# Kernel optimization log

Measured on AMD Instinct MI355X. Metric: run time of the kernel, lower is better.

The kernel has to match this reference:

```python
import jax, jax.numpy as jnp
import numpy as np
from jax import lax

NH = 8  # heads


def _ln(x, g, b):
    m = x.mean(-1, keepdims=True)
    v = ((x - m) ** 2).mean(-1, keepdims=True)
    return (x - m) * lax.rsqrt(v + 1e-5) * g + b


def _pos_idx(n):
    # torch: linspace(n-1,0,n)[:,None] + linspace(0,n-1,n)[None,:], flattened long
    r = np.linspace(n - 1, 0, n).reshape(n, 1)
    c = np.linspace(0, n - 1, n).reshape(1, n)
    return jnp.asarray((r + c).reshape(-1).astype(np.int32))


def _mha(q_in, k_in, v_in, in_w, in_b, out_w, out_b, pos_enc=None, pos_idx=None, attn_mask=None):
    # MultiheadAttentionRelative: q/k/v proj + relative pos-encoding gather terms
    w, bsz, e = q_in.shape
    hd = e // NH
    scale = hd ** -0.5
    q = (q_in @ in_w[:e].T + in_b[:e]) * scale
    k = k_in @ in_w[e:2 * e].T + in_b[e:2 * e]
    v = v_in @ in_w[2 * e:].T + in_b[2 * e:]
    q = q.reshape(w, bsz, NH, hd)
    k = k.reshape(w, bsz, NH, hd)
    v = v.reshape(w, bsz, NH, hd)
    attn = jnp.einsum('wnec,vnec->newv', q, k)  # [N,E,W,W']
    if pos_enc is not None:
        pe = pos_enc[pos_idx].reshape(w, w, e)  # [2W-1,C] -> [W,W',C] gather
        q_r = ((pe @ in_w[:e].T + in_b[:e]) * scale).reshape(w, w, NH, hd)
        k_r = (pe @ in_w[e:2 * e].T + in_b[e:2 * e]).reshape(w, w, NH, hd)
        attn = attn + jnp.einsum('wnec,wvec->newv', q, k_r) + jnp.einsum('vnec,wvec->newv', k, q_r)
    if attn_mask is not None:
        attn = attn + attn_mask[None, None]
    raw = attn
    p = jax.nn.softmax(attn, axis=-1)
    v_o = jnp.einsum('newv,vnec->wnec', p, v).reshape(w, bsz, e)
    return v_o @ out_w.T + out_b, raw.sum(axis=1)


def _interp_lin(x, out_size):
    # torch F.interpolate(mode='linear', align_corners=False) along last axis
    L_in = x.shape[-1]
    if L_in == out_size:
        return x
    coords = jnp.clip((jnp.arange(out_size, dtype=jnp.float32) + 0.5) * (L_in / out_size) - 0.5, 0.0, L_in - 1.0)
    lo = jnp.floor(coords).astype(jnp.int32)
    hi = jnp.minimum(lo + 1, L_in - 1)
    frac = coords - lo.astype(jnp.float32)
    return x[..., lo] * (1.0 - frac) + x[..., hi] * frac


def _conv(x, w, b, pad):
    y = lax.conv_general_dilated(x, w, (1, 1), pad, dimension_numbers=('NCHW', 'OIHW', 'NCHW'))
    return y + b[None, :, None, None]


def _self_layer(feat, feat1, pos, pidx, pos1, pidx1, posy, pidxy, posy1, pidxy1, p):
    iw, ib, ow, ob, n1g, n1b, n2g, n2b = p
    f2 = _ln(feat, n1g, n1b)
    f4 = _ln(feat1, n2g, n2b)
    w_, h2, c = f2.shape
    w1_, h4, c1 = f4.shape
    # row<->col switch: [W,2HN,C] -> [HN,2W,C]
    f2y = jnp.transpose(f2.reshape(w_, 2, h2 // 2, c), (2, 1, 0, 3)).reshape(h2 // 2, 2 * w_, c)
    f4y = jnp.transpose(f4.reshape(w1_, 2, h4 // 2, c1), (2, 1, 0, 3)).reshape(h4 // 2, 2 * w1_, c1)
    f2y, _ = _mha(f2y, f2y, f2y, iw[1], ib[1], ow[1], ob[1], posy, pidxy)
    f2 = jnp.transpose(f2y.reshape(h2 // 2, 2, w_, c), (2, 1, 0, 3)).reshape(w_, h2, c)
    f4y, _ = _mha(f4y, f4y, f4y, iw[3], ib[3], ow[3], ob[3], posy1, pidxy1)
    f4 = jnp.transpose(f4y.reshape(h4 // 2, 2, w1_, c1), (2, 1, 0, 3)).reshape(w1_, h4, c1)
    f2, _ = _mha(f2, f2, f2, iw[0], ib[0], ow[0], ob[0], pos, pidx)
    f4, _ = _mha(f4, f4, f4, iw[2], ib[2], ow[2], ob[2], pos1, pidx1)
    return feat + f2, feat1 + f4


def _cross_layer(fl, fr, fl1, fr1, pos, pidx, pos1, pidx1, p, last):
    iw, ib, ow, ob, n1g, n1b, n2g, n2b, mw1, mb1, mw2, mb2 = p
    fl2 = _ln(fl, n1g, n1b)
    fr2 = _ln(fr, n1g, n1b)
    fl4 = _ln(fl1, n2g, n2b)
    fr4 = _ln(fr1, n2g, n2b)
    up_r, _ = _mha(fr2, fl2, fl2, iw[0], ib[0], ow[0], ob[0], jnp.flip(pos, 0), pidx)
    up_r1, _ = _mha(fr4, fl4, fl4, iw[1], ib[1], ow[1], ob[1], jnp.flip(pos1, 0), pidx1)
    fr = fr + up_r
    fr1n = fr1 + up_r1
    if last:
        w = fl2.shape[0]
        w1 = fl4.shape[0]
        m = jnp.where(jnp.triu(jnp.ones((w, w), jnp.float32), 1) == 1.0, -jnp.inf, 0.0)
        m1 = jnp.where(jnp.triu(jnp.ones((w1, w1), jnp.float32), 1) == 1.0, -jnp.inf, 0.0)
    else:
        m = None
        m1 = None
    fr2n = _ln(fr, n1g, n1b)
    up_l, raw = _mha(fl2, fr2n, fr2n, iw[0], ib[0], ow[0], ob[0], pos, pidx, m)
    fr4n = _ln(fr1n, n2g, n2b)
    up_l1, _ = _mha(fl4, fr4n, fr4n, iw[1], ib[1], ow[1], ob[1], pos1, pidx1, m1)
    fl = fl + up_l
    fl1n = fl1 + up_l1
    feat = jnp.concatenate([fl, fr], 1)        # [W,2HN,C]
    feat_n = jnp.concatenate([fl1n, fr1n], 1)  # [W1,2HN,C]
    x = jnp.transpose(feat_n, (2, 1, 0))       # [C,2HN,W1]
    x = _interp_lin(x, feat.shape[0])          # [C,2HN,W]
    feat_n = jnp.transpose(x, (2, 1, 0))
    feat_n = jnp.concatenate([feat_n, feat], 2)  # [W,2HN,2C]
    x = jnp.transpose(feat_n, (2, 1, 0))[None]   # [1,2C,2HN,W]
    x = _conv(x, mw1, mb1, 'VALID')
    x = _conv(x, mw2, mb2, ((1, 1), (1, 1)))
    out = jnp.transpose(x[0], (2, 1, 0))         # [W,2HN,C]
    return out, raw


def reference(feat_left, feat_right, feat_left1, feat_right1, pos_enc, pos_enc1, pos_enc_y, pos_enc_y1,
              sa_in_w, sa_in_b, sa_out_w, sa_out_b, sa_n1_g, sa_n1_b, sa_n2_g, sa_n2_b,
              ca_in_w, ca_in_b, ca_out_w, ca_out_b, ca_n1_g, ca_n1_b, ca_n2_g, ca_n2_b,
              merge_w1, merge_b1, merge_w2, merge_b2):
    bs, c, h, w = feat_left.shape
    w1 = feat_left1.shape[3]
    hn = h * bs

    def flat(x):
        return jnp.transpose(x, (3, 2, 0, 1)).reshape(x.shape[3], -1, c)  # [W,HN,C]

    fl, fr = flat(feat_left), flat(feat_right)
    fl1, fr1 = flat(feat_left1), flat(feat_right1)
    pidx = _pos_idx(w)
    pidx1 = _pos_idx(w1)
    pidxy = _pos_idx(hn)
    pidxy1 = _pos_idx(hn)
    feat = jnp.concatenate([fl, fr], 1)    # [W,2HN,C]
    feat1 = jnp.concatenate([fl1, fr1], 1)  # [W1,2HN,C]
    L = sa_in_w.shape[0]
    raw = None
    for i in range(L):
        sp = (sa_in_w[i], sa_in_b[i], sa_out_w[i], sa_out_b[i], sa_n1_g[i], sa_n1_b[i], sa_n2_g[i], sa_n2_b[i])
        feat, feat1 = _self_layer(feat, feat1, pos_enc, pidx, pos_enc1, pidx1, pos_enc_y, pidxy, pos_enc_y1, pidxy1, sp)
        cp = (ca_in_w[i], ca_in_b[i], ca_out_w[i], ca_out_b[i], ca_n1_g[i], ca_n1_b[i], ca_n2_g[i], ca_n2_b[i],
              merge_w1[i], merge_b1[i], merge_w2[i], merge_b2[i])
        feat, raw = _cross_layer(feat[:, :hn], feat[:, hn:], feat1[:, :hn], feat1[:, hn:],
                                 pos_enc, pidx, pos_enc1, pidx1, cp, i == L - 1)
    attn_weight = jnp.transpose(raw.reshape(h, bs, w, w), (1, 0, 2, 3))  # [N,H,W,W]
    return attn_weight


def setup_inputs() -> dict:
    key = jax.random.key(0)
    ks = iter(jax.random.split(key, 40))
    N, C, H, W, W1, Lyr = 1, 128, 64, 128, 64, 6
    s = 0.05
    d = {}
    d['feat_left'] = jax.random.normal(next(ks), (N, C, H, W), jnp.float32)
    d['feat_right'] = jax.random.normal(next(ks), (N, C, H, W), jnp.float32)
    d['feat_left1'] = jax.random.normal(next(ks), (N, C, H, W1), jnp.float32)
    d['feat_right1'] = jax.random.normal(next(ks), (N, C, H, W1), jnp.float32)
    d['pos_enc'] = jax.random.normal(next(ks), (2 * W - 1, C), jnp.float32) * 0.1
    d['pos_enc1'] = jax.random.normal(next(ks), (2 * W1 - 1, C), jnp.float32) * 0.1
    d['pos_enc_y'] = jax.random.normal(next(ks), (2 * H - 1, C), jnp.float32) * 0.1
    d['pos_enc_y1'] = jax.random.normal(next(ks), (2 * H - 1, C), jnp.float32) * 0.1
    d['sa_in_w'] = jax.random.normal(next(ks), (Lyr, 4, 3 * C, C), jnp.float32) * s
    d['sa_in_b'] = jnp.zeros((Lyr, 4, 3 * C), jnp.float32)
    d['sa_out_w'] = jax.random.normal(next(ks), (Lyr, 4, C, C), jnp.float32) * s
    d['sa_out_b'] = jnp.zeros((Lyr, 4, C), jnp.float32)
    d['sa_n1_g'] = jnp.ones((Lyr, C), jnp.float32)
    d['sa_n1_b'] = jnp.zeros((Lyr, C), jnp.float32)
    d['sa_n2_g'] = jnp.ones((Lyr, C), jnp.float32)
    d['sa_n2_b'] = jnp.zeros((Lyr, C), jnp.float32)
    d['ca_in_w'] = jax.random.normal(next(ks), (Lyr, 2, 3 * C, C), jnp.float32) * s
    d['ca_in_b'] = jnp.zeros((Lyr, 2, 3 * C), jnp.float32)
    d['ca_out_w'] = jax.random.normal(next(ks), (Lyr, 2, C, C), jnp.float32) * s
    d['ca_out_b'] = jnp.zeros((Lyr, 2, C), jnp.float32)
    d['ca_n1_g'] = jnp.ones((Lyr, C), jnp.float32)
    d['ca_n1_b'] = jnp.zeros((Lyr, C), jnp.float32)
    d['ca_n2_g'] = jnp.ones((Lyr, C), jnp.float32)
    d['ca_n2_b'] = jnp.zeros((Lyr, C), jnp.float32)
    d['merge_w1'] = jax.random.normal(next(ks), (Lyr, 128, 256, 1, 1), jnp.float32) * s
    d['merge_b1'] = jnp.zeros((Lyr, 128), jnp.float32)
    d['merge_w2'] = jax.random.normal(next(ks), (Lyr, 128, 128, 3, 3), jnp.float32) * s
    d['merge_b2'] = jnp.zeros((Lyr, 128), jnp.float32)
    return d
```

## Files before the change

kernel.cpp:

```cpp
#include <hip/hip_runtime.h>
#include <hip/hip_bf16.h>
#include <math.h>


typedef __attribute__((ext_vector_type(8))) short bf16x8;
typedef __attribute__((ext_vector_type(4))) float f32x4;
typedef __hip_bfloat16 bf16;

__device__ __forceinline__ float b2f(unsigned short u) {
  return __uint_as_float((unsigned)u << 16);
}
__device__ __forceinline__ short f2bs(float x) {
  bf16 h = __float2bfloat16(x);
  short s;
  __builtin_memcpy(&s, &h, 2);
  return s;
}
__device__ __forceinline__ int ymap(int t, int D0, int D1) {
  return (t % D0) * (2 * D1) + ((t / D0) & 1) * D1 + t / (2 * D0);
}


__global__ void k_build_feat(const float* __restrict__ L, const float* __restrict__ R,
                             float* __restrict__ feat, int W) {
  int t = blockIdx.x;
  int c = threadIdx.x;
  int b = t & 127;
  int w = t >> 7;
  const float* src = (b < 64) ? L : R;
  int h = b & 63;
  feat[(size_t)t * 128 + c] = src[((size_t)c * 64 + h) * W + w];
}

struct FDesc { const float* s; bf16* d; int n; };
struct FArgs { FDesc d[9]; int cum[10]; int nprob; };
__global__ void k_f2b_multi(FArgs fa) {
  int bid = blockIdx.x;
  int p = 0;
  while (p + 1 < fa.nprob && bid >= fa.cum[p + 1]) ++p;
  const FDesc d = fa.d[p];
  int i = (bid - fa.cum[p]) * 1024 + threadIdx.x * 4;
  if (i + 3 < d.n) {
    float4 x = *(const float4*)(d.s + i);
    d.d[i + 0] = __float2bfloat16(x.x);
    d.d[i + 1] = __float2bfloat16(x.y);
    d.d[i + 2] = __float2bfloat16(x.z);
    d.d[i + 3] = __float2bfloat16(x.w);
  } else {
    for (int z = 0; z < 4 && i + z < d.n; ++z) d.d[i + z] = __float2bfloat16(d.s[i + z]);
  }
}

__global__ void k_wfullb(const float* __restrict__ w2, bf16* __restrict__ wf) {
  int bid = blockIdx.x;
  int l = bid >> 7, co = bid & 127;
  int ci = threadIdx.x;
  const float* src = w2 + (size_t)l * 128 * 128 * 9;
  bf16* dst = wf + (size_t)l * 128 * 1152;
#pragma unroll
  for (int ky = 0; ky < 3; ky++)
#pragma unroll
    for (int kx = 0; kx < 3; kx++)
      dst[(size_t)co * 1152 + (kx * 3 + ky) * 128 + ci] =
          __float2bfloat16(src[((size_t)(co * 128 + ci) * 3 + ky) * 3 + kx]);
}

__global__ void k_zero_guard(bf16* p0, bf16* p1) {
  int t = threadIdx.x;
  p0[255 * 256 + t] = __float2bfloat16(0.0f);
  p1[127 * 256 + t] = __float2bfloat16(0.0f);
}

struct WCArgs { const bf16* iw[12]; const bf16* ow[12]; bf16* out[12]; };
__global__ __launch_bounds__(256) void k_wcomb(WCArgs a) {
  __shared__ bf16 sOw[128 * 128];
  int p = blockIdx.x / 6, rc = blockIdx.x % 6;
  const bf16* iw = a.iw[p];
  const bf16* ow = a.ow[p];
  for (int i = threadIdx.x; i < 128 * 16; i += 256)
    ((bf16x8*)sOw)[i] = ((const bf16x8*)ow)[i];
  __syncthreads();
  int row = rc * 64 + (threadIdx.x >> 2);
  int seg = (threadIdx.x & 3) * 32;
  float acc[32];
#pragma unroll
  for (int c = 0; c < 32; ++c) acc[c] = 0.f;
  for (int t = 0; t < 128; ++t) {
    float av = b2f((unsigned short)iw[row * 128 + t]);
#pragma unroll
    for (int c = 0; c < 32; ++c)
      acc[c] = fmaf(av, b2f((unsigned short)sOw[t * 128 + seg + c]), acc[c]);
  }
  bf16* o = a.out[p] + (size_t)row * 128 + seg;
  for (int c = 0; c < 32; ++c) o[c] = __float2bfloat16(acc[c]);
}

struct BCArgs { const float* iwf[12]; const float* obf[12]; const float* ibf[12]; float* out[12]; };
__global__ void k_bcomb(BCArgs a) {
  int p = blockIdx.x, j = threadIdx.x;
  const float* iw = a.iwf[p] + (size_t)j * 128;
  const float* ob = a.obf[p];
  float acc = a.ibf[p][j];
  for (int t = 0; t < 128; ++t) acc = fmaf(iw[t], ob[t], acc);
  a.out[p][j] = acc;
}


struct LDesc { const float* src; bf16* dst; const float* g; const float* be;
               int ntok, Bout, PBin, offIn; };
struct LArgs { LDesc d[4]; int cum[5]; int nprob; };

__global__ __launch_bounds__(256) void k_ln_multi(LArgs la) {
  int bid = blockIdx.x;
  int p = 0;
  while (p + 1 < la.nprob && bid >= la.cum[p + 1]) ++p;
  const LDesc d = la.d[p];
  int t = (bid - la.cum[p]) * 4 + (threadIdx.x >> 6);
  int lane = threadIdx.x & 63;
  if (t >= d.ntok) return;
  int w = t / d.Bout, b = t - w * d.Bout;
  const float* row = d.src + (size_t)(w * d.PBin + d.offIn + b) * 128;
  float x0 = row[lane], x1 = row[lane + 64];
  float s = x0 + x1;
#pragma unroll
  for (int o = 32; o; o >>= 1) s += __shfl_xor(s, o, 64);
  float m = s * (1.0f / 128.0f);
  float d0 = x0 - m, d1 = x1 - m;
  float v = d0 * d0 + d1 * d1;
#pragma unroll
  for (int o = 32; o; o >>= 1) v += __shfl_xor(v, o, 64);
  float r = 1.0f / sqrtf(v * (1.0f / 128.0f) + 1e-5f);
  bf16* orow = d.dst + (size_t)t * 128;
  orow[lane]      = __float2bfloat16(d0 * r * d.g[lane]      + d.be[lane]);
  orow[lane + 64] = __float2bfloat16(d1 * r * d.g[lane + 64] + d.be[lane + 64]);
}


struct GDesc {
  const bf16* A; const float* Af0; const float* Af1;
  const bf16* W; const float* bias;
  bf16* Cb; float* Cf; const float* resid;
  int M, N, K, lda, scaleN;
  int imode, iD0, iD1;
  int omode, oD0, oD1, ooff;
};
struct GArgs { GDesc d[6]; int cum[7]; int nprob; };

__global__ __launch_bounds__(256) void k_gemm_multi(GArgs ga) {
  __shared__ bf16x8 sA[64 * 4];
  __shared__ bf16x8 sB[64 * 4];
  int bid = blockIdx.x;
  int p = 0;
  while (p + 1 < ga.nprob && bid >= ga.cum[p + 1]) ++p;
  const GDesc d = ga.d[p];
  int local = bid - ga.cum[p];
  int tilesx = d.N >> 6;
  int ty = local / tilesx, tx = local - ty * tilesx;
  const int m0 = ty << 6, n0 = tx << 6;
  const int tid = threadIdx.x;
  const int lane = tid & 63;
  const int wave = tid >> 6;
  const int wm = wave >> 1, wn = wave & 1;
  const int fr = lane & 15;
  const int kc = lane >> 4;
  f32x4 acc[2][2];
#pragma unroll
  for (int f = 0; f < 2; f++)
#pragma unroll
    for (int g = 0; g < 2; g++) acc[f][g] = (f32x4){0.f, 0.f, 0.f, 0.f};

  for (int k0 = 0; k0 < d.K; k0 += 32) {
    {
      int row = tid >> 2, ch = tid & 3;
      int m = m0 + row;
      bf16x8 val = (bf16x8){0, 0, 0, 0, 0, 0, 0, 0};
      if (d.imode == 0) {
        if (m < d.M) val = *(const bf16x8*)(d.A + (size_t)m * d.lda + k0 + ch * 8);
      } else if (d.imode == 1) {
        if (m < d.M) {
          int ar = ymap(m, d.iD0, d.iD1);
          val = *(const bf16x8*)(d.A + (size_t)ar * d.lda + k0 + ch * 8);
        }
      } else if (d.imode == 2) {
        int kblk = k0 >> 7;
        int kx = kblk / 3, ky = kblk - kx * 3;
        int arow = m + (kx - 1) * 128;
        int y = (m & 127) + (ky - 1);
        if (arow >= 0 && arow < d.M && y >= 0 && y < 128)
          val = *(const bf16x8*)(d.A + (size_t)arow * d.lda + (k0 & 127) + ch * 8);
      } else {
        int kk = k0 + ch * 8;
        int w = m >> 7, y = m & 127;
        if (kk < 128) {
          float xo = fminf(fmaxf(w * 0.5f - 0.25f, 0.0f), 63.0f);
          int lo = (int)xo;
          int hi = (lo + 1 < 63) ? lo + 1 : 63;
          float f = xo - (float)lo;
          const float* a0 = d.Af0 + ((size_t)lo * 128 + y) * 128 + kk;
          const float* a1 = d.Af0 + ((size_t)hi * 128 + y) * 128 + kk;
#pragma unroll
          for (int z = 0; z < 8; ++z) val[z] = f2bs(a0[z] * (1.0f - f) + a1[z] * f);
        } else {
          const float* a0 = d.Af1 + (size_t)m * 128 + (kk - 128);
#pragma unroll
          for (int z = 0; z < 8; ++z) val[z] = f2bs(a0[z]);
        }
      }
      sA[row * 4 + (ch ^ ((row >> 2) & 3))] = val;
      bf16x8 bval = *(const bf16x8*)(d.W + (size_t)(n0 + row) * d.K + k0 + ch * 8);
      sB[row * 4 + (ch ^ ((row >> 2) & 3))] = bval;
    }
    __syncthreads();
    bf16x8 af[2], bg[2];
#pragma unroll
    for (int f = 0; f < 2; ++f) {
      int row = wm * 32 + f * 16 + fr;
      af[f] = sA[row * 4 + (kc ^ ((row >> 2) & 3))];
    }
#pragma unroll
    for (int g = 0; g < 2; ++g) {
      int row = wn * 32 + g * 16 + fr;
      bg[g] = sB[row * 4 + (kc ^ ((row >> 2) & 3))];
    }
#pragma unroll
    for (int f = 0; f < 2; ++f)
#pragma unroll
      for (int g = 0; g < 2; ++g)
        acc[f][g] = __builtin_amdgcn_mfma_f32_16x16x32_bf16(af[f], bg[g], acc[f][g], 0, 0, 0);
    __syncthreads();
  }
  const int r4 = (lane >> 4) << 2;
  const int ocol = lane & 15;
#pragma unroll
  for (int f = 0; f < 2; ++f) {
#pragma unroll
    for (int g = 0; g < 2; ++g) {
      int n = n0 + wn * 32 + g * 16 + ocol;
      float bv = d.bias ? d.bias[n] : 0.0f;
      bool sc = (n < d.scaleN);
#pragma unroll
      for (int i = 0; i < 4; ++i) {
        int m = m0 + wm * 32 + f * 16 + r4 + i;
        if (m < d.M) {
          int row;
          if (d.omode == 0) row = (m / d.oD0) * d.oD1 + d.ooff + (m % d.oD0);
          else row = ymap(m, d.oD0, d.oD1);
          size_t idx = (size_t)row * d.N + n;
          float val = acc[f][g][i] + bv;
          if (sc) val *= 0.25f;
          if (d.resid) val += d.resid[idx];
          if (d.Cb) d.Cb[idx] = __float2bfloat16(val);
          else d.Cf[idx] = val;
        }
      }
    }
  }
}


struct ADesc {
  const bf16* Q; const bf16* K; const bf16* V;
  const bf16* PPb; bf16* O;
  int ldQ, ldK, ldV, Wlen, B, sflip, useMask;
};
struct AArgs { ADesc d[2]; int cum[3]; int nprob; };

template<int WLEN, int SGN>
__device__ __forceinline__ void attn_core(const ADesc& d, int b, int st, int h,
                                          int tid, bf16* smem) {
  constexpr int NT = WLEN / 16;
  constexpr int R = WLEN - 1;
  constexpr int PST = WLEN + 8;
  const f32x4 z4 = (f32x4){0.f, 0.f, 0.f, 0.f};
  const bf16x8 zb = (bf16x8){0, 0, 0, 0, 0, 0, 0, 0};
  bf16* Vt  = smem;
  bf16* Pl  = smem + 64 * PST;
  bf16* T2l = smem + 128 * PST;
  bf16* Ost = T2l + 1280;

  {
    int q = tid & (WLEN / 2 - 1);
    int cc = tid >> ((WLEN == 128) ? 6 : 5);
    constexpr int CH = (WLEN == 128) ? 16 : 8;
    int cb = cc * CH;
    const bf16* v0p = d.V + ((size_t)(2 * q) * d.B + b) * d.ldV + h * 64 + cb;
    const bf16* v1p = d.V + ((size_t)(2 * q + 1) * d.B + b) * d.ldV + h * 64 + cb;
#pragma unroll
    for (int j = 0; j < CH; j += 8) {
      bf16x8 a = *(const bf16x8*)(v0p + j);
      bf16x8 bb = *(const bf16x8*)(v1p + j);
#pragma unroll
      for (int z = 0; z < 8; ++z) {
        unsigned pk = (unsigned)(unsigned short)a[z] |
                      ((unsigned)(unsigned short)bb[z] << 16);
        *(unsigned*)(Vt + (size_t)(cb + j + z) * PST + 2 * q) = pk;
      }
    }
  }
  __syncthreads();

  const int wave = tid >> 6, l = tid & 63;
  const int lm = l & 15, lg = l >> 4;
  const bool zlane = (lg >= 2);
  bf16* Pw  = Pl + wave * (16 * PST);
  bf16* T2w = T2l + wave * (16 * 20);
  int p0[4], src[4], hi[4], tsel[4];
  bool csel[4];
#pragma unroll
  for (int i = 0; i < 4; ++i) {
    p0[i] = SGN * (lm - 4 * lg - i) + 15;
    src[i] = (l & 48) | (p0[i] & 15);
    hi[i] = p0[i] & 16;
    if (SGN == 1) {
      int t0 = lm + 15 - 4 * lg - i;
      csel[i] = (t0 < 16);
      tsel[i] = csel[i] ? t0 : t0 - 16;
    } else {
      int t0 = lm - 15 + 4 * lg + i;
      csel[i] = (t0 >= 0);
      tsel[i] = csel[i] ? t0 : t0 + 16;
    }
  }

  const int w0 = st * 16;
  const int chb = h * 64 + wave * 16 + lg * 8;

  bf16x8 qf = zb;
  if (!zlane) qf = *(const bf16x8*)(d.Q + ((size_t)(w0 + lm) * d.B + b) * d.ldQ + chb);

  const int U0 = (SGN == 1) ? (R - w0 - 15) : (R + w0 - WLEN + 1);
  const int Ub0 = (SGN == 1) ? (R - w0 - 15) : (R - (WLEN - 16) + w0 - 15);
  const bf16* t1p = d.PPb + (size_t)(U0 + lm) * 256 + 128 + chb;
  const bf16* t2p = d.PPb + (size_t)(Ub0 + lm) * 256 + chb;
  const int v0i = ((SGN == 1) ? 0 : (WLEN - 16)) + lm;
  const bf16* kp = d.K + ((size_t)v0i * d.B + b) * d.ldK + chb;
  const ptrdiff_t kstep = (ptrdiff_t)SGN * 16 * d.B * d.ldK;

  f32x4 t1a;
  {
    bf16x8 z = zb;
    if (!zlane) z = *(const bf16x8*)t1p;
    t1p += 16 * 256;
    t1a = __builtin_amdgcn_mfma_f32_16x16x32_bf16(qf, z, z4, 0, 0, 0);
  }
  int v = v0i;
#pragma unroll
  for (int j = 0; j < NT; ++j) {
    f32x4 t1b;
    {
      bf16x8 z = zb;
      if (!zlane) z = *(const bf16x8*)t1p;
      t1p += 16 * 256;
      t1b = __builtin_amdgcn_mfma_f32_16x16x32_bf16(qf, z, z4, 0, 0, 0);
    }
    bf16x8 kf = zb;
    if (!zlane) kf = *(const bf16x8*)kp;
    kp += kstep;
    f32x4 s4 = __builtin_amdgcn_mfma_f32_16x16x32_bf16(qf, kf, z4, 0, 0, 0);
    bf16x8 zA = zb, zB = zb;
    if (!zlane) {
      zA = *(const bf16x8*)t2p;
      zB = *(const bf16x8*)(t2p + 16 * 256);
    }
    t2p += 16 * 256;
    f32x4 t2A = __builtin_amdgcn_mfma_f32_16x16x32_bf16(zA, kf, z4, 0, 0, 0);
    f32x4 t2B = __builtin_amdgcn_mfma_f32_16x16x32_bf16(zB, kf, z4, 0, 0, 0);
#pragma unroll
    for (int i = 0; i < 4; ++i)
      T2w[lm * 20 + tsel[i]] = f2bs(csel[i] ? t2A[i] : t2B[i]);
    ushort4 t2u = *(const ushort4*)(T2w + lm * 20 + 4 * lg);
    unsigned short t2a[4] = {t2u.x, t2u.y, t2u.z, t2u.w};
#pragma unroll
    for (int i = 0; i < 4; ++i) {
      float va = __shfl(t1a[i], src[i], 64);
      float vb = __shfl(t1b[i], src[i], 64);
      float s = s4[i] + (hi[i] ? vb : va) + b2f(t2a[i]);
      Pw[(4 * lg + i) * PST + v] = f2bs(__expf(s));
    }
    t1a = t1b;
    v += SGN * 16;
  }
  const bf16x8 ones = (bf16x8){0x3F80, 0x3F80, 0x3F80, 0x3F80,
                               0x3F80, 0x3F80, 0x3F80, 0x3F80};
  f32x4 oa = z4, rsm = z4;
#pragma unroll
  for (int vc = 0; vc < NT / 2; ++vc) {
    bf16x8 pf = *(const bf16x8*)(Pw + lm * PST + vc * 32 + lg * 8);
    bf16x8 vf = *(const bf16x8*)(Vt + (size_t)(wave * 16 + lm) * PST + vc * 32 + lg * 8);
    oa = __builtin_amdgcn_mfma_f32_16x16x32_bf16(pf, vf, oa, 0, 0, 0);
    rsm = __builtin_amdgcn_mfma_f32_16x16x32_bf16(pf, ones, rsm, 0, 0, 0);
  }
#pragma unroll
  for (int i = 0; i < 4; ++i)
    Ost[(4 * lg + i) * 80 + wave * 16 + lm] = f2bs(oa[i] / rsm[i]);
  __syncthreads();
  if (tid < 128) {
    int row = tid >> 3, ch8 = (tid & 7) * 8;
    bf16x8 vv = *(const bf16x8*)(Ost + row * 80 + ch8);
    *(bf16x8*)(d.O + ((size_t)(w0 + row) * d.B + b) * 128 + h * 64 + ch8) = vv;
  }
}

__global__ __launch_bounds__(256, 4) void k_attn_mfma(AArgs aa) {
  extern __shared__ bf16 smem[];
  int bid = blockIdx.x;
  int p = 0;
  while (p + 1 < aa.nprob && bid >= aa.cum[p + 1]) ++p;
  const ADesc d = aa.d[p];
  int local = bid - aa.cum[p];
  int b = local % d.B;
  int rest = local / d.B;
  int ns = d.Wlen >> 4;
  int st = rest % ns, h = rest / ns;
  int tid = threadIdx.x;
  if (d.Wlen == 128) {
    if (d.sflip == 1) attn_core<128, 1>(d, b, st, h, tid, smem);
    else attn_core<128, -1>(d, b, st, h, tid, smem);
  } else {
    if (d.sflip == 1) attn_core<64, 1>(d, b, st, h, tid, smem);
    else attn_core<64, -1>(d, b, st, h, tid, smem);
  }
}

__global__ __launch_bounds__(256, 2) void k_attn_raw(ADesc d) {
  __shared__ bf16 T2l[4 * 16 * 20];
  __shared__ float Rl[4][16][128];
  constexpr int NT = 8;
  constexpr int R = 127;
  const f32x4 z4 = (f32x4){0.f, 0.f, 0.f, 0.f};
  const bf16x8 zb = (bf16x8){0, 0, 0, 0, 0, 0, 0, 0};
  int bid = blockIdx.x;
  int b = bid % d.B, st = bid / d.B;
  int tid = threadIdx.x;
  const int wave = tid >> 6, l = tid & 63;
  const int lm = l & 15, lg = l >> 4;
  const bool zlane = (lg >= 2);
  bf16* T2w = T2l + wave * (16 * 20);
  int p0[4];
#pragma unroll
  for (int i = 0; i < 4; ++i) p0[i] = (lm - 4 * lg - i) + 15;
  const int w0 = st * 16;
  f32x4 raw[NT];
#pragma unroll
  for (int vt = 0; vt < NT; ++vt) raw[vt] = z4;

  for (int hh = 0; hh < 2; ++hh) {
    const int e = wave * 2 + hh;
    const int chb = e * 16 + lg * 8;
    bf16x8 qf = zb;
    if (!zlane) qf = *(const bf16x8*)(d.Q + ((size_t)(w0 + lm) * d.B + b) * d.ldQ + chb);
    const int U0 = R - w0 - 15;
    f32x4 t1a;
    {
      int u = min(max(U0 + lm, 0), 2 * R);
      bf16x8 z = zb;
      if (!zlane) z = *(const bf16x8*)(d.PPb + (size_t)u * 256 + 128 + chb);
      t1a = __builtin_amdgcn_mfma_f32_16x16x32_bf16(qf, z, z4, 0, 0, 0);
    }
#pragma unroll
    for (int j = 0; j < NT; ++j) {
      const int vt = j;
      const int v = vt * 16 + lm;
      f32x4 t1b;
      {
        int u = min(max(U0 + (j + 1) * 16 + lm, 0), 2 * R);
        bf16x8 z = zb;
        if (!zlane) z = *(const bf16x8*)(d.PPb + (size_t)u * 256 + 128 + chb);
        t1b = __builtin_amdgcn_mfma_f32_16x16x32_bf16(qf, z, z4, 0, 0, 0);
      }
      bf16x8 kf = zb;
      if (!zlane) kf = *(const bf16x8*)(d.K + ((size_t)v * d.B + b) * d.ldK + chb);
      f32x4 s4 = __builtin_amdgcn_mfma_f32_16x16x32_bf16(qf, kf, z4, 0, 0, 0);
      const int Ub = R + vt * 16 - w0 - 15;
#pragma unroll
      for (int u2 = 0; u2 < 2; ++u2) {
        int ua = min(max(Ub + u2 * 16 + lm, 0), 2 * R);
        bf16x8 z = zb;
        if (!zlane) z = *(const bf16x8*)(d.PPb + (size_t)ua * 256 + chb);
        f32x4 t2 = __builtin_amdgcn_mfma_f32_16x16x32_bf16(z, kf, z4, 0, 0, 0);
#pragma unroll
        for (int i = 0; i < 4; ++i) {
          int u = Ub + u2 * 16 + 4 * lg + i;
          int t = R + v - u - w0;
          if (t >= 0 && t < 16) T2w[lm * 20 + t] = f2bs(t2[i]);
        }
      }
      ushort4 t2u = *(const ushort4*)(T2w + lm * 20 + 4 * lg);
      unsigned short t2a[4] = {t2u.x, t2u.y, t2u.z, t2u.w};
#pragma unroll
      for (int i = 0; i < 4; ++i) {
        int src = (l & 48) | (p0[i] & 15);
        float va = __shfl(t1a[i], src, 64);
        float vb = __shfl(t1b[i], src, 64);
        float s = s4[i] + ((p0[i] & 16) ? vb : va) + b2f(t2a[i]);
        if (v > (w0 + 4 * lg + i)) s = -INFINITY;
        raw[vt][i] += s;
      }
      t1a = t1b;
    }
  }
#pragma unroll
  for (int vt = 0; vt < NT; ++vt)
#pragma unroll
    for (int i = 0; i < 4; ++i)
      Rl[wave][4 * lg + i][vt * 16 + lm] = raw[vt][i];
  __syncthreads();
  {
    int r = tid >> 4, v8 = (tid & 15) * 8;
    int w = w0 + r;
    bf16* out = d.O + ((size_t)b * 128 + w) * 128;
#pragma unroll
    for (int z = 0; z < 8; ++z) {
      int vv = v8 + z;
      float sum = Rl[0][r][vv] + Rl[1][r][vv] + Rl[2][r][vv] + Rl[3][r][vv];
      out[vv] = __float2bfloat16((vv > w) ? 0.0f : sum);
    }
  }
}


extern "C" void kernel_launch(void* const* d_in, const int* in_sizes, int n_in,
                              void* d_out, int out_size, void* d_ws, size_t ws_size,
                              hipStream_t stream) {
  (void)in_sizes; (void)n_in; (void)out_size; (void)ws_size;
  const float* FLt  = (const float*)d_in[0];
  const float* FRt  = (const float*)d_in[1];
  const float* FL1t = (const float*)d_in[2];
  const float* FR1t = (const float*)d_in[3];
  const float* PE   = (const float*)d_in[4];
  const float* PE1  = (const float*)d_in[5];
  const float* PEY  = (const float*)d_in[6];
  const float* PEY1 = (const float*)d_in[7];
  const float* SA_IW = (const float*)d_in[8];
  const float* SA_IB = (const float*)d_in[9];
  const float* SA_OW = (const float*)d_in[10];
  const float* SA_OB = (const float*)d_in[11];
  const float* SA_N1G = (const float*)d_in[12];
  const float* SA_N1B = (const float*)d_in[13];
  const float* SA_N2G = (const float*)d_in[14];
  const float* SA_N2B = (const float*)d_in[15];
  const float* CA_IW = (const float*)d_in[16];
  const float* CA_IB = (const float*)d_in[17];
  const float* CA_OW = (const float*)d_in[18];
  const float* CA_OB = (const float*)d_in[19];
  const float* CA_N1G = (const float*)d_in[20];
  const float* CA_N1B = (const float*)d_in[21];
  const float* CA_N2G = (const float*)d_in[22];
  const float* CA_N2B = (const float*)d_in[23];
  const float* MW1 = (const float*)d_in[24];
  const float* MB1 = (const float*)d_in[25];
  const float* MW2 = (const float*)d_in[26];
  const float* MB2 = (const float*)d_in[27];

  float* ws = (float*)d_ws;
  float* FEAT  = ws;
  float* FEAT1 = ws + 2097152;
  float* FN2   = ws + 3145728;
  bf16* PP0b   = (bf16*)(ws + 4194304);
  bf16* PP1b   = (bf16*)(ws + 4259840);
  float* B2f   = ws + 4276224;
  bf16* hb = (bf16*)(ws + 4292608);
  bf16* QKV   = hb;
  bf16* QKV1  = hb + 6291456;
  bf16* Xb    = hb + 9437184;
  bf16* XBb   = hb + 11534336;
  bf16* Ob    = hb + 12582912;
  bf16* Ob1   = hb + 14680064;
  bf16* PEb   = hb + 15728640;
  bf16* PE1b  = hb + 15761408;
  bf16* PEYb  = hb + 15777792;
  bf16* PEY1b = hb + 15794176;
  bf16* SAIWb = hb + 15810560;
  bf16* SAOWb = hb + 18169856;
  bf16* CAIWb = hb + 18563072;
  bf16* CAOWb = hb + 19742720;
  bf16* MW1b  = hb + 19939328;
  bf16* WFb   = hb + 20135936;
  bf16* W2b   = hb + 21020672;

  bf16* QR   = QKV + 3145728;
  bf16* FL4F = QKV + 4194304;
  bf16* QR1  = QKV + 5767168;
  bf16* KVq  = QKV1;
  bf16* KVq1 = QKV1 + 2097152;
  bf16* XR2  = Xb;
  bf16* XR21 = Xb + 1048576;

  GArgs ga; int ng = 0; int gb = 0;
  auto gadd = [&](GDesc gd) { ga.cum[ng] = gb; ga.d[ng] = gd;
                              gb += ((gd.M + 63) >> 6) * (gd.N >> 6); ++ng; };
  auto gflush = [&]() { ga.nprob = ng;
                        k_gemm_multi<<<gb, 256, 0, stream>>>(ga); ng = 0; gb = 0; };
  LArgs la; int nl = 0; int lb = 0;
  auto lnadd = [&](LDesc ld) { la.cum[nl] = lb; la.d[nl] = ld;
                               lb += (ld.ntok + 3) / 4; ++nl; };
  auto lnflush = [&]() { la.nprob = nl;
                         k_ln_multi<<<lb, 256, 0, stream>>>(la); nl = 0; lb = 0; };
  AArgs aa; int na = 0; int ab = 0; int maxw = 0;
  auto aadd = [&](ADesc ad) { aa.cum[na] = ab; aa.d[na] = ad;
                              ab += ad.B * (ad.Wlen >> 4) * 2;
                              if (ad.Wlen > maxw) maxw = ad.Wlen; ++na; };
  auto aflush = [&]() { aa.nprob = na;
                        size_t sh = (size_t)(128 * (maxw + 8) + 2560) * 2;
                        k_attn_mfma<<<ab, 256, sh, stream>>>(aa);
                        na = 0; ab = 0; maxw = 0; };

  auto G = [&](const bf16* A, const bf16* W, const float* bias,
               bf16* Cb, float* Cf, const float* resid,
               int M, int N, int K, int lda, int scaleN,
               int imode, int iD0, int iD1,
               int omode, int oD0, int oD1, int ooff,
               const float* Af0 = nullptr, const float* Af1 = nullptr) {
    GDesc gd; gd.A = A; gd.Af0 = Af0; gd.Af1 = Af1; gd.W = W; gd.bias = bias;
    gd.Cb = Cb; gd.Cf = Cf; gd.resid = resid;
    gd.M = M; gd.N = N; gd.K = K; gd.lda = lda; gd.scaleN = scaleN;
    gd.imode = imode; gd.iD0 = iD0; gd.iD1 = iD1;
    gd.omode = omode; gd.oD0 = oD0; gd.oD1 = oD1; gd.ooff = ooff;
    gadd(gd);
  };
  auto AT = [&](const bf16* Q, int ldQ, const bf16* K, int ldK, const bf16* V, int ldV,
                const bf16* PPb, int Wlen, int B, int sflip, bf16* O) {
    ADesc ad; ad.Q = Q; ad.K = K; ad.V = V; ad.PPb = PPb; ad.O = O;
    ad.ldQ = ldQ; ad.ldK = ldK; ad.ldV = ldV; ad.Wlen = Wlen; ad.B = B;
    ad.sflip = sflip; ad.useMask = 0;
    aadd(ad);
  };

  {
    FArgs fa; int nf = 0; int fb = 0;
    auto fadd = [&](const float* s, bf16* dd, int n) {
      fa.cum[nf] = fb; fa.d[nf] = FDesc{s, dd, n}; fb += (n + 1023) / 1024; ++nf; };
    fadd(SA_IW, SAIWb, 6 * 4 * 384 * 128);
    fadd(SA_OW, SAOWb, 6 * 4 * 128 * 128);
    fadd(CA_IW, CAIWb, 6 * 2 * 384 * 128);
    fadd(CA_OW, CAOWb, 6 * 2 * 128 * 128);
    fadd(MW1,   MW1b,  6 * 128 * 256);
    fadd(PE,    PEb,   255 * 128);
    fadd(PE1,   PE1b,  127 * 128);
    fadd(PEY,   PEYb,  127 * 128);
    fadd(PEY1,  PEY1b, 127 * 128);
    fa.nprob = nf;
    k_f2b_multi<<<fb, 256, 0, stream>>>(fa);
  }
  k_wfullb<<<768, 128, 0, stream>>>(MW2, WFb);
  k_zero_guard<<<1, 256, 0, stream>>>(PP0b, PP1b);
  {
    WCArgs wc; BCArgs bc;
    for (int l = 0; l < 6; ++l) {
      for (int s = 0; s < 2; ++s) {
        int p = l * 2 + s;
        int iwi = (s == 0) ? 0 : 2;
        int owi = (s == 0) ? 1 : 3;
        wc.iw[p]  = SAIWb + (size_t)l * 4 * 384 * 128 + (size_t)iwi * 384 * 128;
        wc.ow[p]  = SAOWb + (size_t)l * 4 * 128 * 128 + (size_t)owi * 128 * 128;
        wc.out[p] = W2b + (size_t)p * 384 * 128;
        bc.iwf[p] = SA_IW + (size_t)l * 4 * 384 * 128 + (size_t)iwi * 384 * 128;
        bc.obf[p] = SA_OB + (size_t)l * 4 * 128 + (size_t)owi * 128;
        bc.ibf[p] = SA_IB + (size_t)l * 4 * 384 + (size_t)iwi * 384;
        bc.out[p] = B2f + (size_t)p * 384;
      }
    }
    k_wcomb<<<72, 256, 0, stream>>>(wc);
    k_bcomb<<<12, 384, 0, stream>>>(bc);
  }
  k_build_feat<<<16384, 128, 0, stream>>>(FLt, FRt, FEAT, 128);
  k_build_feat<<<8192, 128, 0, stream>>>(FL1t, FR1t, FEAT1, 64);

  for (int l = 0; l < 6; ++l) {
    bool last = (l == 5);
    const bf16* iw  = SAIWb + (size_t)l * 4 * 384 * 128;
    const float* ib = SA_IB + (size_t)l * 4 * 384;
    const bf16* ow  = SAOWb + (size_t)l * 4 * 128 * 128;
    const float* ob = SA_OB + (size_t)l * 4 * 128;
    const bf16* ciw  = CAIWb + (size_t)l * 2 * 384 * 128;
    const float* cib = CA_IB + (size_t)l * 2 * 384;
    const bf16* cow  = CAOWb + (size_t)l * 2 * 128 * 128;
    const float* cob = CA_OB + (size_t)l * 2 * 128;
    const bf16* ciw1 = ciw + 384 * 128;
    const float* cib1 = cib + 384;
    const bf16* cow1 = cow + 128 * 128;
    const float* cob1 = cob + 128;
    const int IW = 384 * 128, OW = 128 * 128;

    lnadd(LDesc{FEAT, Xb, SA_N1G + l * 128, SA_N1B + l * 128, 16384, 128, 128, 0});
    if (!last) lnadd(LDesc{FEAT1, XBb, SA_N2G + l * 128, SA_N2B + l * 128, 8192, 128, 128, 0});
    lnflush();
    G(Xb, iw + IW, ib + 384, QKV, nullptr, nullptr, 16384, 384, 128, 128, 128, 1, 128, 64, 0, 1, 1, 0);
    if (!last) G(XBb, iw + 3 * IW, ib + 3 * 384, QKV1, nullptr, nullptr, 8192, 384, 128, 128, 128, 1, 64, 64, 0, 1, 1, 0);
    G(PEYb, iw + IW, ib + 384, PP0b, nullptr, nullptr, 127, 256, 128, 128, 128, 0, 0, 0, 0, 1, 1, 0);
    if (!last) G(PEY1b, iw + 3 * IW, ib + 3 * 384, PP1b, nullptr, nullptr, 127, 256, 128, 128, 128, 0, 0, 0, 0, 1, 1, 0);
    gflush();
    AT(QKV, 384, QKV + 128, 384, QKV + 256, 384, PP0b, 64, 256, 1, Ob);
    if (!last) AT(QKV1, 384, QKV1 + 128, 384, QKV1 + 256, 384, PP1b, 64, 128, 1, Ob1);
    aflush();
    G(Ob, W2b + (size_t)(l * 2) * 49152, B2f + (l * 2) * 384, QKV, nullptr, nullptr,
      16384, 384, 128, 128, 128, 1, 64, 128, 0, 1, 1, 0);
    if (!last) G(Ob1, W2b + (size_t)(l * 2 + 1) * 49152, B2f + (l * 2 + 1) * 384, QKV1,
                 nullptr, nullptr, 8192, 384, 128, 128, 128, 1, 64, 64, 0, 1, 1, 0);
    G(PEb, iw, ib, PP0b, nullptr, nullptr, 255, 256, 128, 128, 128, 0, 0, 0, 0, 1, 1, 0);
    if (!last) G(PE1b, iw + 2 * IW, ib + 2 * 384, PP1b, nullptr, nullptr, 127, 256, 128, 128, 128, 0, 0, 0, 0, 1, 1, 0);
    gflush();
    AT(QKV, 384, QKV + 128, 384, QKV + 256, 384, PP0b, 128, 128, 1, Ob);
    if (!last) AT(QKV1, 384, QKV1 + 128, 384, QKV1 + 256, 384, PP1b, 64, 128, 1, Ob1);
    aflush();
    G(Ob, ow, ob, nullptr, FEAT, FEAT, 16384, 128, 128, 128, 0, 0, 0, 0, 0, 1, 1, 0);
    if (!last) G(Ob1, ow + 2 * OW, ob + 2 * 128, nullptr, FEAT1, FEAT1, 8192, 128, 128, 128, 0, 0, 0, 0, 0, 1, 1, 0);
    gflush();

    lnadd(LDesc{FEAT, Xb, CA_N1G + l * 128, CA_N1B + l * 128, 8192, 64, 128, 0});
    lnadd(LDesc{FEAT, Xb + 1048576, CA_N1G + l * 128, CA_N1B + l * 128, 8192, 64, 128, 64});
    if (!last) {
      lnadd(LDesc{FEAT1, XBb, CA_N2G + l * 128, CA_N2B + l * 128, 4096, 64, 128, 0});
      lnadd(LDesc{FEAT1, XBb + 524288, CA_N2G + l * 128, CA_N2B + l * 128, 4096, 64, 128, 64});
    }
    lnflush();
    G(Xb, ciw, cib, QKV, nullptr, nullptr, 8192, 384, 128, 128, 128, 0, 0, 0, 0, 1, 1, 0);
    G(Xb + 1048576, ciw, cib, QR, nullptr, nullptr, 8192, 128, 128, 128, 128, 0, 0, 0, 0, 1, 1, 0);
    if (!last) {
      G(XBb, ciw1, cib1, FL4F, nullptr, nullptr, 4096, 384, 128, 128, 128, 0, 0, 0, 0, 1, 1, 0);
      G(XBb + 524288, ciw1, cib1, QR1, nullptr, nullptr, 4096, 128, 128, 128, 128, 0, 0, 0, 0, 1, 1, 0);
    }
    G(PEb, ciw, cib, PP0b, nullptr, nullptr, 255, 256, 128, 128, 128, 0, 0, 0, 0, 1, 1, 0);
    if (!last) G(PE1b, ciw1, cib1, PP1b, nullptr, nullptr, 127, 256, 128, 128, 128, 0, 0, 0, 0, 1, 1, 0);
    gflush();
    AT(QR, 128, QKV + 128, 384, QKV + 256, 384, PP0b, 128, 64, -1, Ob);
    if (!last) AT(QR1, 128, FL4F + 128, 384, FL4F + 256, 384, PP1b, 64, 64, -1, Ob1);
    aflush();
    G(Ob, cow, cob, nullptr, FEAT, FEAT, 8192, 128, 128, 128, 0, 0, 0, 0, 0, 64, 128, 64);
    if (!last) G(Ob1, cow1, cob1, nullptr, FN2, FEAT1, 4096, 128, 128, 128, 0, 0, 0, 0, 0, 64, 128, 64);
    gflush();
    lnadd(LDesc{FEAT, XR2, CA_N1G + l * 128, CA_N1B + l * 128, 8192, 64, 128, 64});
    if (!last) lnadd(LDesc{FN2, XR21, CA_N2G + l * 128, CA_N2B + l * 128, 4096, 64, 128, 64});
    lnflush();
    G(XR2, ciw + 128 * 128, cib + 128, KVq, nullptr, nullptr, 8192, 256, 128, 128, 0, 0, 0, 0, 0, 1, 1, 0);
    if (!last) G(XR21, ciw1 + 128 * 128, cib1 + 128, KVq1, nullptr, nullptr, 4096, 256, 128, 128, 0, 0, 0, 0, 0, 1, 1, 0);
    gflush();
    if (last) {
      ADesc ad; ad.Q = QKV; ad.K = KVq; ad.V = KVq + 128; ad.PPb = PP0b;
      ad.O = (bf16*)d_out;
      ad.ldQ = 384; ad.ldK = 256; ad.ldV = 256;
      ad.Wlen = 128; ad.B = 64; ad.sflip = 1; ad.useMask = 1;
      k_attn_raw<<<64 * 8, 256, 0, stream>>>(ad);
      break;
    }
    AT(QKV, 384, KVq, 256, KVq + 128, 256, PP0b, 128, 64, 1, Ob);
    AT(FL4F, 384, KVq1, 256, KVq1 + 128, 256, PP1b, 64, 64, 1, Ob1);
    aflush();
    G(Ob, cow, cob, nullptr, FEAT, FEAT, 8192, 128, 128, 128, 0, 0, 0, 0, 0, 64, 128, 0);
    G(Ob1, cow1, cob1, nullptr, FN2, FEAT1, 4096, 128, 128, 128, 0, 0, 0, 0, 0, 64, 128, 0);
    gflush();
    G(nullptr, MW1b + (size_t)l * 128 * 256, MB1 + l * 128, Ob, nullptr, nullptr,
      16384, 128, 256, 256, 0, 3, 0, 0, 0, 1, 1, 0, FN2, FEAT);
    gflush();
    G(Ob, WFb + (size_t)l * 128 * 1152, MB2 + l * 128, nullptr, FEAT, nullptr,
      16384, 128, 1152, 128, 0, 2, 0, 0, 0, 1, 1, 0);
    gflush();
  }
}
```

Measured before the change: 1.593 ms.

## Fuse LayerNorm into GEMM A-operand loading and drop separate LN kernel

Removes the standalone multi-problem LayerNorm kernel and its bf16 intermediate buffers. The GEMM gains a new input mode that computes per-row mean and rstd in shared memory from the fp32 source, then normalizes and converts to bf16 while loading A tiles. This saves kernel launches and a write/read round trip of the normalized activations. In exchange, every N-tile block recomputes the row statistics and rereads the fp32 source, and it uses a one-pass variance formula.

```diff
diff --git a/kernel.cpp b/kernel.cpp
--- a/kernel.cpp
+++ b/kernel.cpp
@@ -106,42 +106,13 @@
 }
 
 
-struct LDesc { const float* src; bf16* dst; const float* g; const float* be;
-               int ntok, Bout, PBin, offIn; };
-struct LArgs { LDesc d[4]; int cum[5]; int nprob; };
-
-__global__ __launch_bounds__(256) void k_ln_multi(LArgs la) {
-  int bid = blockIdx.x;
-  int p = 0;
-  while (p + 1 < la.nprob && bid >= la.cum[p + 1]) ++p;
-  const LDesc d = la.d[p];
-  int t = (bid - la.cum[p]) * 4 + (threadIdx.x >> 6);
-  int lane = threadIdx.x & 63;
-  if (t >= d.ntok) return;
-  int w = t / d.Bout, b = t - w * d.Bout;
-  const float* row = d.src + (size_t)(w * d.PBin + d.offIn + b) * 128;
-  float x0 = row[lane], x1 = row[lane + 64];
-  float s = x0 + x1;
-#pragma unroll
-  for (int o = 32; o; o >>= 1) s += __shfl_xor(s, o, 64);
-  float m = s * (1.0f / 128.0f);
-  float d0 = x0 - m, d1 = x1 - m;
-  float v = d0 * d0 + d1 * d1;
-#pragma unroll
-  for (int o = 32; o; o >>= 1) v += __shfl_xor(v, o, 64);
-  float r = 1.0f / sqrtf(v * (1.0f / 128.0f) + 1e-5f);
-  bf16* orow = d.dst + (size_t)t * 128;
-  orow[lane]      = __float2bfloat16(d0 * r * d.g[lane]      + d.be[lane]);
-  orow[lane + 64] = __float2bfloat16(d1 * r * d.g[lane + 64] + d.be[lane + 64]);
-}
-
-
 struct GDesc {
   const bf16* A; const float* Af0; const float* Af1;
   const bf16* W; const float* bias;
   bf16* Cb; float* Cf; const float* resid;
+  const float* lnsrc; const float* lng; const float* lnbe;
   int M, N, K, lda, scaleN;
-  int imode, iD0, iD1;
+  int imode, iD0, iD1, lnOff, lnYmap;
   int omode, oD0, oD1, ooff;
 };
 struct GArgs { GDesc d[6]; int cum[7]; int nprob; };
@@ -149,6 +120,8 @@
 __global__ __launch_bounds__(256) void k_gemm_multi(GArgs ga) {
   __shared__ bf16x8 sA[64 * 4];
   __shared__ bf16x8 sB[64 * 4];
+  __shared__ float sMean[64];
+  __shared__ float sRstd[64];
   int bid = blockIdx.x;
   int p = 0;
   while (p + 1 < ga.nprob && bid >= ga.cum[p + 1]) ++p;
@@ -163,6 +136,31 @@
   const int wm = wave >> 1, wn = wave & 1;
   const int fr = lane & 15;
   const int kc = lane >> 4;
+
+  if (d.imode == 5) {
+    int row = tid >> 2, q = tid & 3;
+    int m = m0 + row;
+    int r = d.lnYmap ? ymap(m, d.iD0, d.iD1)
+                     : (m / d.iD0) * d.iD1 + d.lnOff + (m % d.iD0);
+    const float* src = d.lnsrc + (size_t)r * 128 + q * 32;
+    float s = 0.f, ss = 0.f;
+#pragma unroll
+    for (int j = 0; j < 32; j += 4) {
+      float4 x = *(const float4*)(src + j);
+      s += x.x + x.y + x.z + x.w;
+      ss += x.x * x.x + x.y * x.y + x.z * x.z + x.w * x.w;
+    }
+    s += __shfl_xor(s, 1, 64); s += __shfl_xor(s, 2, 64);
+    ss += __shfl_xor(ss, 1, 64); ss += __shfl_xor(ss, 2, 64);
+    if (q == 0) {
+      float mean = s * (1.0f / 128.0f);
+      float var = fmaxf(ss * (1.0f / 128.0f) - mean * mean, 0.0f);
+      sMean[row] = mean;
+      sRstd[row] = 1.0f / sqrtf(var + 1e-5f);
+    }
+    __syncthreads();
+  }
+
   f32x4 acc[2][2];
 #pragma unroll
   for (int f = 0; f < 2; f++)
@@ -188,6 +186,16 @@
         int y = (m & 127) + (ky - 1);
         if (arow >= 0 && arow < d.M && y >= 0 && y < 128)
           val = *(const bf16x8*)(d.A + (size_t)arow * d.lda + (k0 & 127) + ch * 8);
+      } else if (d.imode == 5) {
+        int r = d.lnYmap ? ymap(m, d.iD0, d.iD1)
+                         : (m / d.iD0) * d.iD1 + d.lnOff + (m % d.iD0);
+        const float* a0 = d.lnsrc + (size_t)r * 128 + k0 + ch * 8;
+        const float* gg = d.lng + k0 + ch * 8;
+        const float* bb = d.lnbe + k0 + ch * 8;
+        float mean = sMean[row], rstd = sRstd[row];
+#pragma unroll
+        for (int z = 0; z < 8; ++z)
+          val[z] = f2bs((a0[z] - mean) * rstd * gg[z] + bb[z]);
       } else {
         int kk = k0 + ch * 8;
         int w = m >> 7, y = m & 127;
@@ -562,8 +570,6 @@
   bf16* hb = (bf16*)(ws + 4292608);
   bf16* QKV   = hb;
   bf16* QKV1  = hb + 6291456;
-  bf16* Xb    = hb + 9437184;
-  bf16* XBb   = hb + 11534336;
   bf16* Ob    = hb + 12582912;
   bf16* Ob1   = hb + 14680064;
   bf16* PEb   = hb + 15728640;
@@ -583,19 +589,12 @@
   bf16* QR1  = QKV + 5767168;
   bf16* KVq  = QKV1;
   bf16* KVq1 = QKV1 + 2097152;
-  bf16* XR2  = Xb;
-  bf16* XR21 = Xb + 1048576;
 
   GArgs ga; int ng = 0; int gb = 0;
   auto gadd = [&](GDesc gd) { ga.cum[ng] = gb; ga.d[ng] = gd;
                               gb += ((gd.M + 63) >> 6) * (gd.N >> 6); ++ng; };
   auto gflush = [&]() { ga.nprob = ng;
                         k_gemm_multi<<<gb, 256, 0, stream>>>(ga); ng = 0; gb = 0; };
-  LArgs la; int nl = 0; int lb = 0;
-  auto lnadd = [&](LDesc ld) { la.cum[nl] = lb; la.d[nl] = ld;
-                               lb += (ld.ntok + 3) / 4; ++nl; };
-  auto lnflush = [&]() { la.nprob = nl;
-                         k_ln_multi<<<lb, 256, 0, stream>>>(la); nl = 0; lb = 0; };
   AArgs aa; int na = 0; int ab = 0; int maxw = 0;
   auto aadd = [&](ADesc ad) { aa.cum[na] = ab; aa.d[na] = ad;
                               ab += ad.B * (ad.Wlen >> 4) * 2;
@@ -613,9 +612,25 @@
                const float* Af0 = nullptr, const float* Af1 = nullptr) {
     GDesc gd; gd.A = A; gd.Af0 = Af0; gd.Af1 = Af1; gd.W = W; gd.bias = bias;
     gd.Cb = Cb; gd.Cf = Cf; gd.resid = resid;
+    gd.lnsrc = nullptr; gd.lng = nullptr; gd.lnbe = nullptr;
+    gd.lnOff = 0; gd.lnYmap = 0;
     gd.M = M; gd.N = N; gd.K = K; gd.lda = lda; gd.scaleN = scaleN;
     gd.imode = imode; gd.iD0 = iD0; gd.iD1 = iD1;
     gd.omode = omode; gd.oD0 = oD0; gd.oD1 = oD1; gd.ooff = ooff;
+    gadd(gd);
+  };
+  auto GL = [&](const float* lnsrc, const float* lng, const float* lnbe,
+                int lnYmap, int iD0, int iD1, int lnOff,
+                const bf16* W, const float* bias, bf16* Cb,
+                int M, int N, int scaleN) {
+    GDesc gd; gd.A = nullptr; gd.Af0 = nullptr; gd.Af1 = nullptr;
+    gd.W = W; gd.bias = bias;
+    gd.Cb = Cb; gd.Cf = nullptr; gd.resid = nullptr;
+    gd.lnsrc = lnsrc; gd.lng = lng; gd.lnbe = lnbe;
+    gd.lnOff = lnOff; gd.lnYmap = lnYmap;
+    gd.M = M; gd.N = N; gd.K = 128; gd.lda = 128; gd.scaleN = scaleN;
+    gd.imode = 5; gd.iD0 = iD0; gd.iD1 = iD1;
+    gd.omode = 0; gd.oD0 = 1; gd.oD1 = 1; gd.ooff = 0;
     gadd(gd);
   };
   auto AT = [&](const bf16* Q, int ldQ, const bf16* K, int ldK, const bf16* V, int ldV,
@@ -681,12 +696,13 @@
     const bf16* cow1 = cow + 128 * 128;
     const float* cob1 = cob + 128;
     const int IW = 384 * 128, OW = 128 * 128;
-
-    lnadd(LDesc{FEAT, Xb, SA_N1G + l * 128, SA_N1B + l * 128, 16384, 128, 128, 0});
-    if (!last) lnadd(LDesc{FEAT1, XBb, SA_N2G + l * 128, SA_N2B + l * 128, 8192, 128, 128, 0});
-    lnflush();
-    G(Xb, iw + IW, ib + 384, QKV, nullptr, nullptr, 16384, 384, 128, 128, 128, 1, 128, 64, 0, 1, 1, 0);
-    if (!last) G(XBb, iw + 3 * IW, ib + 3 * 384, QKV1, nullptr, nullptr, 8192, 384, 128, 128, 128, 1, 64, 64, 0, 1, 1, 0);
+    const float* n1g = SA_N1G + l * 128; const float* n1b = SA_N1B + l * 128;
+    const float* n2g = SA_N2G + l * 128; const float* n2b = SA_N2B + l * 128;
+    const float* c1g = CA_N1G + l * 128; const float* c1b = CA_N1B + l * 128;
+    const float* c2g = CA_N2G + l * 128; const float* c2b = CA_N2B + l * 128;
+
+    GL(FEAT, n1g, n1b, 1, 128, 64, 0, iw + IW, ib + 384, QKV, 16384, 384, 128);
+    if (!last) GL(FEAT1, n2g, n2b, 1, 64, 64, 0, iw + 3 * IW, ib + 3 * 384, QKV1, 8192, 384, 128);
     G(PEYb, iw + IW, ib + 384, PP0b, nullptr, nullptr, 127, 256, 128, 128, 128, 0, 0, 0, 0, 1, 1, 0);
     if (!last) G(PEY1b, iw + 3 * IW, ib + 3 * 384, PP1b, nullptr, nullptr, 127, 256, 128, 128, 128, 0, 0, 0, 0, 1, 1, 0);
     gflush();
@@ -707,18 +723,11 @@
     if (!last) G(Ob1, ow + 2 * OW, ob + 2 * 128, nullptr, FEAT1, FEAT1, 8192, 128, 128, 128, 0, 0, 0, 0, 0, 1, 1, 0);
     gflush();
 
-    lnadd(LDesc{FEAT, Xb, CA_N1G + l * 128, CA_N1B + l * 128, 8192, 64, 128, 0});
-    lnadd(LDesc{FEAT, Xb + 1048576, CA_N1G + l * 128, CA_N1B + l * 128, 8192, 64, 128, 64});
+    GL(FEAT, c1g, c1b, 0, 64, 128, 0, ciw, cib, QKV, 8192, 384, 128);
+    GL(FEAT, c1g, c1b, 0, 64, 128, 64, ciw, cib, QR, 8192, 128, 128);
     if (!last) {
-      lnadd(LDesc{FEAT1, XBb, CA_N2G + l * 128, CA_N2B + l * 128, 4096, 64, 128, 0});
-      lnadd(LDesc{FEAT1, XBb + 524288, CA_N2G + l * 128, CA_N2B + l * 128, 4096, 64, 128, 64});
-    }
-    lnflush();
-    G(Xb, ciw, cib, QKV, nullptr, nullptr, 8192, 384, 128, 128, 128, 0, 0, 0, 0, 1, 1, 0);
-    G(Xb + 1048576, ciw, cib, QR, nullptr, nullptr, 8192, 128, 128, 128, 128, 0, 0, 0, 0, 1, 1, 0);
-    if (!last) {
-      G(XBb, ciw1, cib1, FL4F, nullptr, nullptr, 4096, 384, 128, 128, 128, 0, 0, 0, 0, 1, 1, 0);
-      G(XBb + 524288, ciw1, cib1, QR1, nullptr, nullptr, 4096, 128, 128, 128, 128, 0, 0, 0, 0, 1, 1, 0);
+      GL(FEAT1, c2g, c2b, 0, 64, 128, 0, ciw1, cib1, FL4F, 4096, 384, 128);
+      GL(FEAT1, c2g, c2b, 0, 64, 128, 64, ciw1, cib1, QR1, 4096, 128, 128);
     }
     G(PEb, ciw, cib, PP0b, nullptr, nullptr, 255, 256, 128, 128, 128, 0, 0, 0, 0, 1, 1, 0);
     if (!last) G(PE1b, ciw1, cib1, PP1b, nullptr, nullptr, 127, 256, 128, 128, 128, 0, 0, 0, 0, 1, 1, 0);
@@ -729,11 +738,8 @@
     G(Ob, cow, cob, nullptr, FEAT, FEAT, 8192, 128, 128, 128, 0, 0, 0, 0, 0, 64, 128, 64);
     if (!last) G(Ob1, cow1, cob1, nullptr, FN2, FEAT1, 4096, 128, 128, 128, 0, 0, 0, 0, 0, 64, 128, 64);
     gflush();
-    lnadd(LDesc{FEAT, XR2, CA_N1G + l * 128, CA_N1B + l * 128, 8192, 64, 128, 64});
-    if (!last) lnadd(LDesc{FN2, XR21, CA_N2G + l * 128, CA_N2B + l * 128, 4096, 64, 128, 64});
-    lnflush();
-    G(XR2, ciw + 128 * 128, cib + 128, KVq, nullptr, nullptr, 8192, 256, 128, 128, 0, 0, 0, 0, 0, 1, 1, 0);
-    if (!last) G(XR21, ciw1 + 128 * 128, cib1 + 128, KVq1, nullptr, nullptr, 4096, 256, 128, 128, 0, 0, 0, 0, 0, 1, 1, 0);
+    GL(FEAT, c1g, c1b, 0, 64, 128, 64, ciw + 128 * 128, cib + 128, KVq, 8192, 256, 0);
+    if (!last) GL(FN2, c2g, c2b, 0, 64, 128, 64, ciw1 + 128 * 128, cib1 + 128, KVq1, 4096, 256, 0);
     gflush();
     if (last) {
       ADesc ad; ad.Q = QKV; ad.K = KVq; ad.V = KVq + 128; ad.PPb = PP0b;
```

Measured after the change: 1.642 ms. +3.1%, slower.
